# Kernel optimization log

Hardware: AMD Instinct MI355X
Metric: run time of the kernel (lower is better)

The kernel has to match this reference:

```python
import jax, jax.numpy as jnp
import numpy as np

NUM_ITEMS = 50000
B = 512      # batch of (user, item) pairs
L = 50       # padded per-user item-list length
K = 20       # top_k: length of each context channel
H = 32       # hidden_dim
D = 32       # output_dim


def setup_inputs() -> dict:
    key = jax.random.key(0)
    ks = jax.random.split(key, 8)
    ctx = jax.random.normal(ks[0], (NUM_ITEMS, 10, K), dtype=jnp.float32)
    item_idxs = jax.random.randint(ks[1], (B,), 0, NUM_ITEMS)
    user_items = jax.random.randint(ks[2], (B, L), 0, NUM_ITEMS)
    user_lens = jax.random.randint(ks[3], (B,), 1, L + 1)  # ragged lengths in [1, L]
    W1 = jax.random.normal(ks[4], (5, 1, H), dtype=jnp.float32) * 0.1
    b1 = jnp.zeros((5, H), dtype=jnp.float32)
    W2 = jax.random.normal(ks[5], (5, H, D), dtype=jnp.float32) * 0.1
    b2 = jnp.zeros((5, D), dtype=jnp.float32)
    Wout = jax.random.normal(ks[6], (D, 1), dtype=jnp.float32) * 0.1
    bout = jnp.zeros((1,), dtype=jnp.float32)
    return dict(ctx=ctx, W1=W1, b1=b1, W2=W2, b2=b2, Wout=Wout, bout=bout,
                item_idxs=item_idxs, user_items=user_items, user_lens=user_lens)


def _item_rep(feat, W1, b1, W2, b2):
    """feat: [..., 10, K] context channels -> [..., 5*K, D] item representation.
    Channels (2c, 2c+1) go through com_{c+1}: a shared 1->H->D MLP applied to each
    scalar (unsqueeze(1) in the original), outputs of the two channels multiplied."""
    prefix = feat.shape[:-2]
    x = feat.reshape(prefix + (5, 2, K))                     # [..., 5, 2, K]
    w1 = W1[:, 0, :].reshape((5, 1, 1, H))                   # input_dim == 1
    h = jax.nn.relu(x[..., None] * w1 + b1.reshape((5, 1, 1, H)))   # [..., 5, 2, K, H]
    o = jnp.einsum('...cpkh,chd->...cpkd', h, W2) + b2.reshape((5, 1, 1, D))
    rep = o[..., 0, :, :] * o[..., 1, :, :]                  # [..., 5, K, D]
    return rep.reshape(prefix + (5 * K, D))


def reference(ctx, W1, b1, W2, b2, Wout, bout, item_idxs, user_items, user_lens):
    # Target-item representations: gather contexts then tiny MLPs. [B, 5K, D]
    item_rep = _item_rep(ctx[item_idxs], W1, b1, W2, b2)
    # Per-user item reps (padded ragged) and masked mean over the item list.
    u_rep = _item_rep(ctx[user_items], W1, b1, W2, b2)       # [B, L, 5K, D]
    mask = (jnp.arange(L)[None, :] < user_lens[:, None]).astype(u_rep.dtype)  # [B, L]
    u_mean = jnp.einsum('blnd,bl->bnd', u_rep, mask) / user_lens[:, None, None].astype(u_rep.dtype)
    inter = u_mean * item_rep                                # [B, 5K, D]
    pred = jax.nn.sigmoid(inter @ Wout + bout)               # [B, 5K, 1]
    return pred.reshape(B * 5 * K, 1)
```

## Files before the change

### kernel.cpp

```cpp
#include <hip/hip_runtime.h>
#include <math.h>

#define NITEMS 50000
#define BATCH  512
#define LLEN   50
#define KTOP   20
#define HDIM   32
#define DDIM   32
#define NCH    5
#define NSEG   33
#define NSCAL  200
#define NCELL  100
#define THRP   33
#define NWAVE  8
#define CSLOT  13

typedef _Float16 h2 __attribute__((ext_vector_type(2)));

static __device__ __forceinline__ float dot2_acc(h2 a, h2 b, float c) {
#if __has_builtin(__builtin_amdgcn_fdot2)
    return __builtin_amdgcn_fdot2(a, b, c, false);
#else
    return fmaf((float)a.x, (float)b.x, fmaf((float)a.y, (float)b.y, c));
#endif
}

#define WS_THRS  0
#define WS_AB16  160
#define WS_ORDER 5440


__global__ __launch_bounds__(256) void cnn_setup(
        const float* __restrict__ W1, const float* __restrict__ b1,
        const float* __restrict__ W2, const float* __restrict__ b2,
        const int* __restrict__ user_lens,
        float* __restrict__ ws, int* __restrict__ order) {
    const int tid = threadIdx.x;

    if (blockIdx.x < NSEG) {
        __shared__ float sW1[NCH*HDIM], sB1[NCH*HDIM], sThr[NCH*HDIM];
        __shared__ int   sRank[NCH*HDIM];
        __shared__ float sW2[NCH*HDIM*DDIM];
        __shared__ float sB2[NCH*DDIM];

        for (int i = tid; i < NCH*HDIM; i += 256) { sW1[i] = W1[i]; sB1[i] = b1[i]; }
        for (int i = tid; i < NCH*HDIM*DDIM; i += 256) sW2[i] = W2[i];
        for (int i = tid; i < NCH*DDIM; i += 256) sB2[i] = b2[i];
        __syncthreads();

        for (int i = tid; i < NCH*HDIM; i += 256) {
            float w = sW1[i];
            sThr[i] = (w != 0.f) ? (-sB1[i] / w) : INFINITY;
        }
        __syncthreads();

        for (int i = tid; i < NCH*HDIM; i += 256) {
            int c = i / HDIM, h = i % HDIM;
            float thr = sThr[i];
            int rank = 0;
            for (int h2i = 0; h2i < HDIM; ++h2i) {
                float thr2 = sThr[c*HDIM + h2i];
                rank += (thr2 < thr || (thr2 == thr && h2i < h)) ? 1 : 0;
            }
            sRank[i] = rank;
            if (blockIdx.x == 0) ws[WS_THRS + c*HDIM + rank] = thr;
        }
        __syncthreads();

        const int s = blockIdx.x;
        if (tid < NCH*DDIM) {
            int c = tid / DDIM, d = tid % DDIM;
            float A = 0.f, Bv = 0.f;
#pragma unroll
            for (int h = 0; h < HDIM; ++h) {
                float w  = sW1[c*HDIM + h];
                float bb = sB1[c*HDIM + h];
                int   r  = sRank[c*HDIM + h];
                bool active = (w > 0.f) ? (r < s) : ((w < 0.f) ? (r >= s) : (bb > 0.f));
                if (active) {
                    float w2 = sW2[(c*HDIM + h)*DDIM + d];
                    A  = fmaf(w,  w2, A);
                    Bv = fmaf(bb, w2, Bv);
                }
            }
            Bv += sB2[c*DDIM + d];
            unsigned short* ab = (unsigned short*)(ws + WS_AB16);
            int d4 = d >> 2, dd = d & 3;
            int base = ((c*NSEG + s)*32 + d4*4)*2;
            _Float16 ah = (_Float16)A, bh = (_Float16)Bv;
            ab[base + 4*(dd>>1) + (dd&1)]     = __builtin_bit_cast(unsigned short, ah);
            ab[base + 4*(dd>>1) + 2 + (dd&1)] = __builtin_bit_cast(unsigned short, bh);
        }
    } else {
        __shared__ int sHist[LLEN + 1];
        for (int i = tid; i <= LLEN; i += 256) sHist[i] = 0;
        __syncthreads();
        for (int i = tid; i < BATCH; i += 256) atomicAdd(&sHist[user_lens[i]], 1);
        __syncthreads();
        if (tid == 0) {
            int accum = 0;
            for (int l = 1; l <= LLEN; ++l) { int c = sHist[l]; sHist[l] = accum; accum += c; }
        }
        __syncthreads();
        for (int i = tid; i < BATCH; i += 256) {
            int pos = atomicAdd(&sHist[user_lens[i]], 1);
            order[pos] = i;
        }
    }
}

__global__ __launch_bounds__(512, 4) void cnn_main(
        const float* __restrict__ ctx,  const float* __restrict__ ws,
        const float* __restrict__ Wout, const float* __restrict__ bout,
        const int* __restrict__ item_idxs, const int* __restrict__ user_items,
        const int* __restrict__ user_lens, const int* __restrict__ order,
        float* __restrict__ out) {
    __shared__ unsigned int sAB16[NCH*NSEG*32];
    __shared__ float  sThrS[NCH*THRP];
    __shared__ uint2  sxo[NWAVE][NCELL];
    __shared__ uint2  sWt[NCELL*8];
    __shared__ float  pRed[NWAVE][NCELL];

    const int tid  = threadIdx.x;
    const int w    = tid >> 6;
    const int lane = tid & 63;
    const int g    = lane >> 3;
    const int d4   = lane & 7;

    const uint4* ABg = reinterpret_cast<const uint4*>(ws + WS_AB16);
    uint4* sAB4 = reinterpret_cast<uint4*>(sAB16);
    for (int i = tid; i < NCH*NSEG*8; i += 512) sAB4[i] = ABg[i];
    for (int i = tid; i < NCH*THRP; i += 512) {
        int c = i / THRP, j = i - c*THRP;
        sThrS[i] = (j < HDIM) ? ws[WS_THRS + c*HDIM + j] : 0.f;
    }

    const int rank = (blockIdx.x < 256) ? blockIdx.x : (767 - blockIdx.x);
    const int b    = order[rank];
    const int len  = user_lens[b];
    const float inv_len = 1.f / (float)len;
    const float bo = bout[0];
    const h2 wv0 = {(_Float16)Wout[4*d4],     (_Float16)Wout[4*d4 + 1]};
    const h2 wv1 = {(_Float16)Wout[4*d4 + 2], (_Float16)Wout[4*d4 + 3]};

    int sc[4], sdst[4];
#pragma unroll
    for (int r = 0; r < 4; ++r) {
        int idx  = lane + 64*r;
        int c    = idx / 40, rr = idx - c*40;
        int cell = c*KTOP + (rr % KTOP);
        sc[r]   = c;
        sdst[r] = cell*8 + (rr / KTOP)*4;
    }

    const int nstripe = (len > w) ? ((len - w + NWAVE - 1) / NWAVE) : 0;

    unsigned int wtA[CSLOT], wtB[CSLOT];
    float acc[CSLOT];
#pragma unroll
    for (int i = 0; i < CSLOT; ++i) acc[i] = 0.f;

    char* sxoB = (char*)&sxo[w][0];

    __syncthreads();

    float xp[4] = {0.f, 0.f, 0.f, 0.f};
    if (nstripe > 0) {
        const float* row = ctx + (size_t)user_items[b*LLEN + w] * NSCAL;
#pragma unroll
        for (int r = 0; r < 4; ++r) {
            int idx = lane + 64*r;
            if (idx < NSCAL) xp[r] = row[idx];
        }
    }

    if (w == 0) {
        float xt[4] = {0.f, 0.f, 0.f, 0.f};
        const float* row = ctx + (size_t)item_idxs[b] * NSCAL;
#pragma unroll
        for (int r = 0; r < 4; ++r) {
            int idx = lane + 64*r;
            if (idx < NSCAL) xt[r] = row[idx];
        }
#pragma unroll
        for (int r = 0; r < 4; ++r) {
            int idx = lane + 64*r;
            if (idx < NSCAL) {
                float xv = xt[r];
                int base = sc[r]*THRP;
                int pos = 0;
                pos += (sThrS[base + pos + 15] < xv) ? 16 : 0;
                pos += (sThrS[base + pos + 7]  < xv) ? 8  : 0;
                pos += (sThrS[base + pos + 3]  < xv) ? 4  : 0;
                pos += (sThrS[base + pos + 1]  < xv) ? 2  : 0;
                pos += (sThrS[base + pos]      < xv) ? 1  : 0;
                unsigned int off = (unsigned int)((sc[r]*NSEG + pos) << 7);
                _Float16 xh = (_Float16)xv;
                unsigned int word = (unsigned int)__builtin_bit_cast(unsigned short, xh)
                                  | (off << 16);
                *(unsigned int*)(sxoB + sdst[r]) = word;
            }
        }
        __builtin_amdgcn_wave_barrier();
#pragma unroll
        for (int i = 0; i < CSLOT; ++i) {
            int cell = g + 8*i;
            if (cell < NCELL) {
                uint2 xo = sxo[0][cell];
                const uint4* p0 = (const uint4*)((const char*)sAB16 + (xo.x >> 16) + (d4 << 4));
                const uint4* p1 = (const uint4*)((const char*)sAB16 + (xo.y >> 16) + (d4 << 4));
                uint4 q0 = *p0, q1 = *p1;
                _Float16 x0h = __builtin_bit_cast(_Float16, (unsigned short)(xo.x & 0xffffu));
                _Float16 x1h = __builtin_bit_cast(_Float16, (unsigned short)(xo.y & 0xffffu));
                h2 x0 = {x0h, x0h}, x1 = {x1h, x1h};
                h2 repa = (x0 * __builtin_bit_cast(h2, q0.x) + __builtin_bit_cast(h2, q0.y))
                        * (x1 * __builtin_bit_cast(h2, q1.x) + __builtin_bit_cast(h2, q1.y));
                h2 repb = (x0 * __builtin_bit_cast(h2, q0.z) + __builtin_bit_cast(h2, q0.w))
                        * (x1 * __builtin_bit_cast(h2, q1.z) + __builtin_bit_cast(h2, q1.w));
                wtA[i] = __builtin_bit_cast(unsigned int, (h2)(repa * wv0));
                wtB[i] = __builtin_bit_cast(unsigned int, (h2)(repb * wv1));
                sWt[cell*8 + d4] = make_uint2(wtA[i], wtB[i]);
            }
        }
    }
    __syncthreads();

    if (w != 0) {
#pragma unroll
        for (int i = 0; i < CSLOT; ++i) {
            int cell = g + 8*i;
            if (cell < NCELL) {
                uint2 v = sWt[cell*8 + d4];
                wtA[i] = v.x; wtB[i] = v.y;
            }
        }
    }

    for (int j = 0; j < nstripe; ++j) {
        float xc[4];
#pragma unroll
        for (int r = 0; r < 4; ++r) xc[r] = xp[r];

        if (j + 1 < nstripe) {
            const float* row = ctx + (size_t)user_items[b*LLEN + w + NWAVE*(j+1)] * NSCAL;
#pragma unroll
            for (int r = 0; r < 4; ++r) {
                int idx = lane + 64*r;
                if (idx < NSCAL) xp[r] = row[idx];
            }
        }

#pragma unroll
        for (int r = 0; r < 4; ++r) {
            int idx = lane + 64*r;
            if (idx < NSCAL) {
                float xv = xc[r];
                int base = sc[r]*THRP;
                int pos = 0;
                pos += (sThrS[base + pos + 15] < xv) ? 16 : 0;
                pos += (sThrS[base + pos + 7]  < xv) ? 8  : 0;
                pos += (sThrS[base + pos + 3]  < xv) ? 4  : 0;
                pos += (sThrS[base + pos + 1]  < xv) ? 2  : 0;
                pos += (sThrS[base + pos]      < xv) ? 1  : 0;
                unsigned int off = (unsigned int)((sc[r]*NSEG + pos) << 7);
                _Float16 xh = (_Float16)xv;
                unsigned int word = (unsigned int)__builtin_bit_cast(unsigned short, xh)
                                  | (off << 16);
                *(unsigned int*)(sxoB + sdst[r]) = word;
            }
        }
        __builtin_amdgcn_wave_barrier();

#pragma unroll
        for (int i = 0; i < CSLOT; ++i) {
            int cell = g + 8*i;
            if (cell < NCELL) {
                uint2 xo = sxo[w][cell];
                const uint4* p0 = (const uint4*)((const char*)sAB16 + (xo.x >> 16) + (d4 << 4));
                const uint4* p1 = (const uint4*)((const char*)sAB16 + (xo.y >> 16) + (d4 << 4));
                uint4 q0 = *p0, q1 = *p1;
                _Float16 x0h = __builtin_bit_cast(_Float16, (unsigned short)(xo.x & 0xffffu));
                _Float16 x1h = __builtin_bit_cast(_Float16, (unsigned short)(xo.y & 0xffffu));
                h2 x0 = {x0h, x0h}, x1 = {x1h, x1h};
                h2 repa = (x0 * __builtin_bit_cast(h2, q0.x) + __builtin_bit_cast(h2, q0.y))
                        * (x1 * __builtin_bit_cast(h2, q1.x) + __builtin_bit_cast(h2, q1.y));
                h2 repb = (x0 * __builtin_bit_cast(h2, q0.z) + __builtin_bit_cast(h2, q0.w))
                        * (x1 * __builtin_bit_cast(h2, q1.z) + __builtin_bit_cast(h2, q1.w));
                acc[i] = dot2_acc(repa, __builtin_bit_cast(h2, wtA[i]),
                         dot2_acc(repb, __builtin_bit_cast(h2, wtB[i]), acc[i]));
            }
        }
        __builtin_amdgcn_wave_barrier();
    }

#pragma unroll
    for (int i = 0; i < CSLOT; ++i) {
        int cell = g + 8*i;
        float v = acc[i];
        v += __shfl_xor(v, 1, 64);
        v += __shfl_xor(v, 2, 64);
        v += __shfl_xor(v, 4, 64);
        if (d4 == 0 && cell < NCELL) pRed[w][cell] = v;
    }
    __syncthreads();
    if (tid < NCELL) {
        float p = 0.f;
#pragma unroll
        for (int q = 0; q < NWAVE; ++q) p += pRed[q][tid];
        out[b*NCELL + tid] = 1.f / (1.f + expf(-(p*inv_len + bo)));
    }
}

extern "C" void kernel_launch(void* const* d_in, const int* in_sizes, int n_in,
                              void* d_out, int out_size, void* d_ws, size_t ws_size,
                              hipStream_t stream) {
    const float* ctx   = (const float*)d_in[0];
    const float* W1    = (const float*)d_in[1];
    const float* b1    = (const float*)d_in[2];
    const float* W2    = (const float*)d_in[3];
    const float* b2    = (const float*)d_in[4];
    const float* Wout  = (const float*)d_in[5];
    const float* bout  = (const float*)d_in[6];
    const int* item_idxs  = (const int*)d_in[7];
    const int* user_items = (const int*)d_in[8];
    const int* user_lens  = (const int*)d_in[9];
    float* out = (float*)d_out;
    float* ws  = (float*)d_ws;
    int*   order = (int*)(ws + WS_ORDER);

    cnn_setup<<<NSEG + 1, 256, 0, stream>>>(W1, b1, W2, b2, user_lens, ws, order);
    cnn_main<<<BATCH, 512, 0, stream>>>(ctx, ws, Wout, bout,
                                        item_idxs, user_items, user_lens,
                                        order, out);
}
```

Before: 115.8 us.

## Fuse setup kernel into main kernel, recomputing tables and sort order per block

Removes the separate setup launch: each main block now loads W1/b1, computes the ReLU thresholds and ranks, builds the fp16 segment coefficient tables in shared memory, and builds a length histogram to find its own batch index by rank. This drops a kernel launch and the global workspace round-trip. In exchange, every one of the 512 blocks repeats the setup work (about 5K dot products over W2 read from global/L2) before its main loop, which lengthens each block's prologue.

```diff
diff --git a/kernel.cpp b/kernel.cpp
--- a/kernel.cpp
+++ b/kernel.cpp
@@ -25,95 +25,13 @@
 #endif
 }
 
-#define WS_THRS  0
-#define WS_AB16  160
-#define WS_ORDER 5440
-
-
-__global__ __launch_bounds__(256) void cnn_setup(
-        const float* __restrict__ W1, const float* __restrict__ b1,
-        const float* __restrict__ W2, const float* __restrict__ b2,
-        const int* __restrict__ user_lens,
-        float* __restrict__ ws, int* __restrict__ order) {
-    const int tid = threadIdx.x;
-
-    if (blockIdx.x < NSEG) {
-        __shared__ float sW1[NCH*HDIM], sB1[NCH*HDIM], sThr[NCH*HDIM];
-        __shared__ int   sRank[NCH*HDIM];
-        __shared__ float sW2[NCH*HDIM*DDIM];
-        __shared__ float sB2[NCH*DDIM];
-
-        for (int i = tid; i < NCH*HDIM; i += 256) { sW1[i] = W1[i]; sB1[i] = b1[i]; }
-        for (int i = tid; i < NCH*HDIM*DDIM; i += 256) sW2[i] = W2[i];
-        for (int i = tid; i < NCH*DDIM; i += 256) sB2[i] = b2[i];
-        __syncthreads();
-
-        for (int i = tid; i < NCH*HDIM; i += 256) {
-            float w = sW1[i];
-            sThr[i] = (w != 0.f) ? (-sB1[i] / w) : INFINITY;
-        }
-        __syncthreads();
-
-        for (int i = tid; i < NCH*HDIM; i += 256) {
-            int c = i / HDIM, h = i % HDIM;
-            float thr = sThr[i];
-            int rank = 0;
-            for (int h2i = 0; h2i < HDIM; ++h2i) {
-                float thr2 = sThr[c*HDIM + h2i];
-                rank += (thr2 < thr || (thr2 == thr && h2i < h)) ? 1 : 0;
-            }
-            sRank[i] = rank;
-            if (blockIdx.x == 0) ws[WS_THRS + c*HDIM + rank] = thr;
-        }
-        __syncthreads();
-
-        const int s = blockIdx.x;
-        if (tid < NCH*DDIM) {
-            int c = tid / DDIM, d = tid % DDIM;
-            float A = 0.f, Bv = 0.f;
-#pragma unroll
-            for (int h = 0; h < HDIM; ++h) {
-                float w  = sW1[c*HDIM + h];
-                float bb = sB1[c*HDIM + h];
-                int   r  = sRank[c*HDIM + h];
-                bool active = (w > 0.f) ? (r < s) : ((w < 0.f) ? (r >= s) : (bb > 0.f));
-                if (active) {
-                    float w2 = sW2[(c*HDIM + h)*DDIM + d];
-                    A  = fmaf(w,  w2, A);
-                    Bv = fmaf(bb, w2, Bv);
-                }
-            }
-            Bv += sB2[c*DDIM + d];
-            unsigned short* ab = (unsigned short*)(ws + WS_AB16);
-            int d4 = d >> 2, dd = d & 3;
-            int base = ((c*NSEG + s)*32 + d4*4)*2;
-            _Float16 ah = (_Float16)A, bh = (_Float16)Bv;
-            ab[base + 4*(dd>>1) + (dd&1)]     = __builtin_bit_cast(unsigned short, ah);
-            ab[base + 4*(dd>>1) + 2 + (dd&1)] = __builtin_bit_cast(unsigned short, bh);
-        }
-    } else {
-        __shared__ int sHist[LLEN + 1];
-        for (int i = tid; i <= LLEN; i += 256) sHist[i] = 0;
-        __syncthreads();
-        for (int i = tid; i < BATCH; i += 256) atomicAdd(&sHist[user_lens[i]], 1);
-        __syncthreads();
-        if (tid == 0) {
-            int accum = 0;
-            for (int l = 1; l <= LLEN; ++l) { int c = sHist[l]; sHist[l] = accum; accum += c; }
-        }
-        __syncthreads();
-        for (int i = tid; i < BATCH; i += 256) {
-            int pos = atomicAdd(&sHist[user_lens[i]], 1);
-            order[pos] = i;
-        }
-    }
-}
-
 __global__ __launch_bounds__(512, 4) void cnn_main(
-        const float* __restrict__ ctx,  const float* __restrict__ ws,
+        const float* __restrict__ ctx,
+        const float* __restrict__ W1g, const float* __restrict__ b1g,
+        const float* __restrict__ W2g, const float* __restrict__ b2g,
         const float* __restrict__ Wout, const float* __restrict__ bout,
         const int* __restrict__ item_idxs, const int* __restrict__ user_items,
-        const int* __restrict__ user_lens, const int* __restrict__ order,
+        const int* __restrict__ user_lens,
         float* __restrict__ out) {
     __shared__ unsigned int sAB16[NCH*NSEG*32];
     __shared__ float  sThrS[NCH*THRP];
@@ -127,16 +45,99 @@
     const int g    = lane >> 3;
     const int d4   = lane & 7;
 
-    const uint4* ABg = reinterpret_cast<const uint4*>(ws + WS_AB16);
-    uint4* sAB4 = reinterpret_cast<uint4*>(sAB16);
-    for (int i = tid; i < NCH*NSEG*8; i += 512) sAB4[i] = ABg[i];
-    for (int i = tid; i < NCH*THRP; i += 512) {
-        int c = i / THRP, j = i - c*THRP;
-        sThrS[i] = (j < HDIM) ? ws[WS_THRS + c*HDIM + j] : 0.f;
-    }
-
     const int rank = (blockIdx.x < 256) ? blockIdx.x : (767 - blockIdx.x);
-    const int b    = order[rank];
+
+    float* sW1f  = &pRed[0][0];
+    float* sB1f  = sW1f + NCH*HDIM;
+    float* sThrT = sB1f + NCH*HDIM;
+    int*   sRank = (int*)(sThrT + NCH*HDIM);
+    int*   sBp   = sRank + NCH*HDIM;
+    int*   sHist = (int*)&sWt[0];
+
+    for (int i = tid; i < NCH*HDIM; i += 512) { sW1f[i] = W1g[i]; sB1f[i] = b1g[i]; }
+    if (tid <= LLEN) sHist[tid] = 0;
+    if (tid == 0) *sBp = rank;
+    __syncthreads();
+
+    for (int i = tid; i < NCH*HDIM; i += 512) {
+        float wv = sW1f[i];
+        sThrT[i] = (wv != 0.f) ? (-sB1f[i] / wv) : INFINITY;
+    }
+    atomicAdd(&sHist[user_lens[tid]], 1);
+    __syncthreads();
+
+    for (int i = tid; i < NCH*HDIM; i += 512) {
+        int c = i >> 5, h = i & 31;
+        float thr = sThrT[i];
+        int rnk = 0;
+        for (int hh = 0; hh < HDIM; ++hh) {
+            float t2 = sThrT[(c<<5) + hh];
+            rnk += (t2 < thr || (t2 == thr && hh < h)) ? 1 : 0;
+        }
+        sRank[i] = rnk;
+        sThrS[c*THRP + rnk] = thr;
+    }
+    if (tid == 0) {
+        int accum = 0;
+        for (int l = 1; l <= LLEN; ++l) { int cc = sHist[l]; sHist[l] = accum; accum += cc; }
+    }
+    __syncthreads();
+
+    {
+        unsigned short* ab = (unsigned short*)sAB16;
+        for (int e = tid; e < NCH*NSEG*DDIM; e += 512) {
+            int d  = e & 31;
+            int cs = e >> 5;
+            int c  = cs / NSEG, s = cs - c*NSEG;
+            float A = 0.f, Bv = 0.f;
+#pragma unroll
+            for (int h = 0; h < HDIM; ++h) {
+                float wv = sW1f[(c<<5) + h];
+                float bb = sB1f[(c<<5) + h];
+                int   r  = sRank[(c<<5) + h];
+                bool active = (wv > 0.f) ? (r < s) : ((wv < 0.f) ? (r >= s) : (bb > 0.f));
+                if (active) {
+                    float w2 = W2g[((c<<5) + h)*DDIM + d];
+                    A  = fmaf(wv, w2, A);
+                    Bv = fmaf(bb, w2, Bv);
+                }
+            }
+            Bv += b2g[(c<<5) + d];
+            int dq = d >> 2, dd = d & 3;
+            int base = ((c*NSEG + s)*32 + dq*4)*2;
+            _Float16 ah = (_Float16)A, bh = (_Float16)Bv;
+            ab[base + 4*(dd>>1) + (dd&1)]     = __builtin_bit_cast(unsigned short, ah);
+            ab[base + 4*(dd>>1) + 2 + (dd&1)] = __builtin_bit_cast(unsigned short, bh);
+        }
+    }
+    __syncthreads();
+
+    if (w == 0) {
+        int l = lane;
+        bool inb = (l >= 1 && l <= LLEN) && (sHist[l] <= rank)
+                && (l == LLEN || sHist[l+1] > rank);
+        unsigned long long mm = __ballot(inb);
+        if (mm != 0ull) {
+            int lstar = (int)__builtin_ctzll(mm);
+            int need = rank - sHist[lstar];
+            if (need < 0) need = 0;
+            for (int chunk = 0; chunk < BATCH/64; ++chunk) {
+                int j = (chunk << 6) + lane;
+                unsigned long long mb = __ballot(user_lens[j] == lstar);
+                int cnt = __popcll(mb);
+                if (need < cnt) {
+                    if (((mb >> lane) & 1ull) &&
+                        __popcll(mb & ((1ull << lane) - 1ull)) == need)
+                        *sBp = j;
+                    break;
+                }
+                need -= cnt;
+            }
+        }
+    }
+    __syncthreads();
+
+    const int b    = (*sBp) & (BATCH - 1);
     const int len  = user_lens[b];
     const float inv_len = 1.f / (float)len;
     const float bo = bout[0];
@@ -161,8 +162,6 @@
     for (int i = 0; i < CSLOT; ++i) acc[i] = 0.f;
 
     char* sxoB = (char*)&sxo[w][0];
-
-    __syncthreads();
 
     float xp[4] = {0.f, 0.f, 0.f, 0.f};
     if (nstripe > 0) {
@@ -325,11 +324,8 @@
     const int* user_items = (const int*)d_in[8];
     const int* user_lens  = (const int*)d_in[9];
     float* out = (float*)d_out;
-    float* ws  = (float*)d_ws;
-    int*   order = (int*)(ws + WS_ORDER);
-
-    cnn_setup<<<NSEG + 1, 256, 0, stream>>>(W1, b1, W2, b2, user_lens, ws, order);
-    cnn_main<<<BATCH, 512, 0, stream>>>(ctx, ws, Wout, bout,
-                                        item_idxs, user_items, user_lens,
-                                        order, out);
+    (void)d_ws; (void)ws_size;
+
+    cnn_main<<<BATCH, 512, 0, stream>>>(ctx, W1, b1, W2, b2, Wout, bout,
+                                        item_idxs, user_items, user_lens, out);
 }
```

Result: slower. 170.7 us (+47.4%).

## Split each batch row across two blocks by top-k halves

Applied to the files above, without the earlier changes.

Each block now handles half of the 100 output cells (10 of the 20 top-k positions per channel) for one batch row, and the grid doubles to 1024 blocks. Per-thread register arrays shrink from 13 to 7 slots and launch bounds request 8 blocks per CU, aiming for more parallelism and occupancy on the ragged user-length workload. In exchange, both blocks fetch the user_items indices, the target-item work and the shared-table staging separately, and each reads only half of every ctx row, so global loads are less contiguous.

```diff
diff --git a/kernel.cpp b/kernel.cpp
--- a/kernel.cpp
+++ b/kernel.cpp
@@ -11,9 +11,10 @@
 #define NSEG   33
 #define NSCAL  200
 #define NCELL  100
+#define NCELLH 50
 #define THRP   33
 #define NWAVE  8
-#define CSLOT  13
+#define CSLOTH 7
 
 typedef _Float16 h2 __attribute__((ext_vector_type(2)));
 
@@ -109,7 +110,7 @@
     }
 }
 
-__global__ __launch_bounds__(512, 4) void cnn_main(
+__global__ __launch_bounds__(512, 8) void cnn_main(
         const float* __restrict__ ctx,  const float* __restrict__ ws,
         const float* __restrict__ Wout, const float* __restrict__ bout,
         const int* __restrict__ item_idxs, const int* __restrict__ user_items,
@@ -117,9 +118,9 @@
         float* __restrict__ out) {
     __shared__ unsigned int sAB16[NCH*NSEG*32];
     __shared__ float  sThrS[NCH*THRP];
-    __shared__ uint2  sxo[NWAVE][NCELL];
-    __shared__ uint2  sWt[NCELL*8];
-    __shared__ float  pRed[NWAVE][NCELL];
+    __shared__ uint2  sxo[NWAVE][NCELLH];
+    __shared__ uint2  sWt[NCELLH*8];
+    __shared__ float  pRed[NWAVE][NCELLH];
 
     const int tid  = threadIdx.x;
     const int w    = tid >> 6;
@@ -135,7 +136,9 @@
         sThrS[i] = (j < HDIM) ? ws[WS_THRS + c*HDIM + j] : 0.f;
     }
 
-    const int rank = (blockIdx.x < 256) ? blockIdx.x : (767 - blockIdx.x);
+    const int rowSlot = blockIdx.x >> 1;
+    const int half    = blockIdx.x & 1;
+    const int rank = (rowSlot < 256) ? rowSlot : (767 - rowSlot);
     const int b    = order[rank];
     const int len  = user_lens[b];
     const float inv_len = 1.f / (float)len;
@@ -143,49 +146,50 @@
     const h2 wv0 = {(_Float16)Wout[4*d4],     (_Float16)Wout[4*d4 + 1]};
     const h2 wv1 = {(_Float16)Wout[4*d4 + 2], (_Float16)Wout[4*d4 + 3]};
 
-    int sc[4], sdst[4];
-#pragma unroll
-    for (int r = 0; r < 4; ++r) {
-        int idx  = lane + 64*r;
-        int c    = idx / 40, rr = idx - c*40;
-        int cell = c*KTOP + (rr % KTOP);
-        sc[r]   = c;
-        sdst[r] = cell*8 + (rr / KTOP)*4;
+    int sc[2], sdst[2], sgi[2];
+#pragma unroll
+    for (int r = 0; r < 2; ++r) {
+        int lidx = lane + 64*r;
+        int c    = lidx / 20, rr = lidx - c*20;
+        int slot = rr / 10,  kk = rr - slot*10;
+        sc[r]   = (lidx < 100) ? c : 0;
+        sdst[r] = (c*10 + kk)*8 + slot*4;
+        sgi[r]  = c*40 + slot*20 + half*10 + kk;
     }
 
     const int nstripe = (len > w) ? ((len - w + NWAVE - 1) / NWAVE) : 0;
 
-    unsigned int wtA[CSLOT], wtB[CSLOT];
-    float acc[CSLOT];
-#pragma unroll
-    for (int i = 0; i < CSLOT; ++i) acc[i] = 0.f;
+    unsigned int wtA[CSLOTH], wtB[CSLOTH];
+    float acc[CSLOTH];
+#pragma unroll
+    for (int i = 0; i < CSLOTH; ++i) acc[i] = 0.f;
 
     char* sxoB = (char*)&sxo[w][0];
 
     __syncthreads();
 
-    float xp[4] = {0.f, 0.f, 0.f, 0.f};
+    float xp[2] = {0.f, 0.f};
     if (nstripe > 0) {
         const float* row = ctx + (size_t)user_items[b*LLEN + w] * NSCAL;
 #pragma unroll
-        for (int r = 0; r < 4; ++r) {
-            int idx = lane + 64*r;
-            if (idx < NSCAL) xp[r] = row[idx];
+        for (int r = 0; r < 2; ++r) {
+            int lidx = lane + 64*r;
+            if (lidx < 100) xp[r] = row[sgi[r]];
         }
     }
 
     if (w == 0) {
-        float xt[4] = {0.f, 0.f, 0.f, 0.f};
+        float xt[2] = {0.f, 0.f};
         const float* row = ctx + (size_t)item_idxs[b] * NSCAL;
 #pragma unroll
-        for (int r = 0; r < 4; ++r) {
-            int idx = lane + 64*r;
-            if (idx < NSCAL) xt[r] = row[idx];
-        }
-#pragma unroll
-        for (int r = 0; r < 4; ++r) {
-            int idx = lane + 64*r;
-            if (idx < NSCAL) {
+        for (int r = 0; r < 2; ++r) {
+            int lidx = lane + 64*r;
+            if (lidx < 100) xt[r] = row[sgi[r]];
+        }
+#pragma unroll
+        for (int r = 0; r < 2; ++r) {
+            int lidx = lane + 64*r;
+            if (lidx < 100) {
                 float xv = xt[r];
                 int base = sc[r]*THRP;
                 int pos = 0;
@@ -203,9 +207,9 @@
         }
         __builtin_amdgcn_wave_barrier();
 #pragma unroll
-        for (int i = 0; i < CSLOT; ++i) {
+        for (int i = 0; i < CSLOTH; ++i) {
             int cell = g + 8*i;
-            if (cell < NCELL) {
+            if (cell < NCELLH) {
                 uint2 xo = sxo[0][cell];
                 const uint4* p0 = (const uint4*)((const char*)sAB16 + (xo.x >> 16) + (d4 << 4));
                 const uint4* p1 = (const uint4*)((const char*)sAB16 + (xo.y >> 16) + (d4 << 4));
@@ -227,9 +231,9 @@
 
     if (w != 0) {
 #pragma unroll
-        for (int i = 0; i < CSLOT; ++i) {
+        for (int i = 0; i < CSLOTH; ++i) {
             int cell = g + 8*i;
-            if (cell < NCELL) {
+            if (cell < NCELLH) {
                 uint2 v = sWt[cell*8 + d4];
                 wtA[i] = v.x; wtB[i] = v.y;
             }
@@ -237,23 +241,23 @@
     }
 
     for (int j = 0; j < nstripe; ++j) {
-        float xc[4];
-#pragma unroll
-        for (int r = 0; r < 4; ++r) xc[r] = xp[r];
+        float xc[2];
+#pragma unroll
+        for (int r = 0; r < 2; ++r) xc[r] = xp[r];
 
         if (j + 1 < nstripe) {
             const float* row = ctx + (size_t)user_items[b*LLEN + w + NWAVE*(j+1)] * NSCAL;
 #pragma unroll
-            for (int r = 0; r < 4; ++r) {
-                int idx = lane + 64*r;
-                if (idx < NSCAL) xp[r] = row[idx];
-            }
-        }
-
-#pragma unroll
-        for (int r = 0; r < 4; ++r) {
-            int idx = lane + 64*r;
-            if (idx < NSCAL) {
+            for (int r = 0; r < 2; ++r) {
+                int lidx = lane + 64*r;
+                if (lidx < 100) xp[r] = row[sgi[r]];
+            }
+        }
+
+#pragma unroll
+        for (int r = 0; r < 2; ++r) {
+            int lidx = lane + 64*r;
+            if (lidx < 100) {
                 float xv = xc[r];
                 int base = sc[r]*THRP;
                 int pos = 0;
@@ -272,9 +276,9 @@
         __builtin_amdgcn_wave_barrier();
 
 #pragma unroll
-        for (int i = 0; i < CSLOT; ++i) {
+        for (int i = 0; i < CSLOTH; ++i) {
             int cell = g + 8*i;
-            if (cell < NCELL) {
+            if (cell < NCELLH) {
                 uint2 xo = sxo[w][cell];
                 const uint4* p0 = (const uint4*)((const char*)sAB16 + (xo.x >> 16) + (d4 << 4));
                 const uint4* p1 = (const uint4*)((const char*)sAB16 + (xo.y >> 16) + (d4 << 4));
@@ -294,20 +298,21 @@
     }
 
 #pragma unroll
-    for (int i = 0; i < CSLOT; ++i) {
+    for (int i = 0; i < CSLOTH; ++i) {
         int cell = g + 8*i;
         float v = acc[i];
         v += __shfl_xor(v, 1, 64);
         v += __shfl_xor(v, 2, 64);
         v += __shfl_xor(v, 4, 64);
-        if (d4 == 0 && cell < NCELL) pRed[w][cell] = v;
+        if (d4 == 0 && cell < NCELLH) pRed[w][cell] = v;
     }
     __syncthreads();
-    if (tid < NCELL) {
+    if (tid < NCELLH) {
         float p = 0.f;
 #pragma unroll
         for (int q = 0; q < NWAVE; ++q) p += pRed[q][tid];
-        out[b*NCELL + tid] = 1.f / (1.f + expf(-(p*inv_len + bo)));
+        int cellG = (tid / 10)*KTOP + half*10 + (tid % 10);
+        out[b*NCELL + cellG] = 1.f / (1.f + expf(-(p*inv_len + bo)));
     }
 }
 
@@ -329,7 +334,7 @@
     int*   order = (int*)(ws + WS_ORDER);
 
     cnn_setup<<<NSEG + 1, 256, 0, stream>>>(W1, b1, W2, b2, user_lens, ws, order);
-    cnn_main<<<BATCH, 512, 0, stream>>>(ctx, ws, Wout, bout,
-                                        item_idxs, user_items, user_lens,
-                                        order, out);
+    cnn_main<<<2*BATCH, 512, 0, stream>>>(ctx, ws, Wout, bout,
+                                          item_idxs, user_items, user_lens,
+                                          order, out);
 }
```

Result: faster. 112.9 us (-2.6%).
